# Performance work log

Measured on AMD Instinct MI355X. Metric: run time of the kernel, lower is better.

The kernel has to match this reference:

```python
import jax, jax.numpy as jnp
import numpy as np

B, CIN, COUT, S1, S2, M1, M2 = 16, 64, 64, 128, 128, 16, 16


def _cas(L, dtype):
    # Hartley 'cas' matrix: cos(2*pi*k*k'/L) + sin(2*pi*k*k'/L), symmetric LxL
    k = jnp.arange(L, dtype=dtype)
    ang = (2.0 * jnp.pi / L) * (k[:, None] * k[None, :])
    return jnp.cos(ang) + jnp.sin(ang)


def dht2(x):
    # x: [B, C, M, N] -> dense 2D discrete Hartley transform via matmuls
    M, N = x.shape[-2], x.shape[-1]
    cas_row = _cas(M, x.dtype)
    cas_col = _cas(N, x.dtype)
    # torch: matmul(x, cas_col.T) then matmul(cas_row.T, .)
    y = jnp.einsum('bimn,gn->bimg', x, cas_col)
    return jnp.einsum('mf,bimn->bifn', cas_row, y)


def idht2(x):
    return dht2(x) / (x.shape[-2] * x.shape[-1])


def _neg_freq(a):
    # roll(flip(a, [-1,-2]), (1,1), [-1,-2])
    return jnp.roll(jnp.flip(a, axis=(-2, -1)), shift=(1, 1), axis=(-2, -1))


def compl_mul2d(x1, x2):
    x1n = _neg_freq(x1)
    x2n = _neg_freq(x2)
    e = lambda a, b: jnp.einsum('bixy,ioxy->boxy', a, b)
    return 0.5 * (e(x1, x2) - e(x1n, x2n) + e(x1, x2n) + e(x1n, x2))


def setup_inputs() -> dict:
    key = jax.random.key(0)
    k1, k2, k3 = jax.random.split(key, 3)
    scale = 1.0 / (CIN * COUT)
    x = jax.random.normal(k1, (B, CIN, S1, S2), dtype=jnp.float32)
    weights1 = scale * jax.random.uniform(k2, (CIN, COUT, M1, M2), dtype=jnp.float32)
    weights2 = scale * jax.random.uniform(k3, (CIN, COUT, M1, M2), dtype=jnp.float32)
    return {'x': x, 'weights1': weights1, 'weights2': weights2}


def reference(x, weights1, weights2):
    m1, m2 = weights1.shape[2], weights1.shape[3]
    b, cout = x.shape[0], weights1.shape[1]
    s1, s2 = x.shape[-2], x.shape[-1]

    cos_part = dht2(x)
    sin_part = dht2(jnp.flip(x, axis=(-2, -1)))
    # torch.angle(complex(cos, sin)) == atan2(sin, cos)
    phase = jnp.arctan2(sin_part, cos_part)

    out_dht = jnp.zeros((b, cout, s1, s2), dtype=x.dtype)
    out_dht = out_dht.at[:, :, :m1, :m2].set(
        compl_mul2d(cos_part[:, :, :m1, :m2], weights1))
    out_dht = out_dht.at[:, :, -m1:, :m2].set(
        compl_mul2d(cos_part[:, :, -m1:, :m2], weights2))

    y = idht2(out_dht)
    return y * jnp.cos(phase)
```

## Files before the change

kernel.cpp:

```cpp
#include <hip/hip_runtime.h>

typedef _Float16 f16;
typedef f16 f16x4 __attribute__((ext_vector_type(4)));
typedef f16 f16x8 __attribute__((ext_vector_type(8)));
typedef float f32x4 __attribute__((ext_vector_type(4)));

#define LSCALE 2048.0f
#define LINV   4.8828125e-4f
#define XS 140
#define CS 137

#define MFMA(A,B,C) __builtin_amdgcn_mfma_f32_16x16x32_f16(A, B, C, 0, 0, 0)

__global__ void k_cas(float* __restrict__ casf,
                      f16* __restrict__ Ah, f16* __restrict__ Al,
                      f16* __restrict__ Vh, f16* __restrict__ Vl) {
    int f = blockIdx.x, m = threadIdx.x;
    const float SC = (float)(6.283185307179586 / 128.0);
    float ang = SC * (float)(f * m);
    double a = (double)ang;
    float v = (float)cos(a) + (float)sin(a);
    casf[f * 128 + m] = v;
    f16 h = (f16)v;
    f16 lo = (f16)((v - (float)h) * LSCALE);
    Ah[f * 128 + m] = h;
    Al[f * 128 + m] = lo;
    Vh[f * 128 + 127 - m] = h;
    Vl[f * 128 + 127 - m] = lo;
}

__global__ __launch_bounds__(512, 2) void k_dht(
    const float* __restrict__ xg,
    const f16* __restrict__ Ah, const f16* __restrict__ Al,
    const f16* __restrict__ Vh, const f16* __restrict__ Vl,
    float* __restrict__ cosphi,
    float* __restrict__ cp1, float* __restrict__ cp2)
{
    __shared__ __align__(16) char smem[143360];
    f16* Xh  = (f16*)smem;
    f16* Xl  = (f16*)(smem + 35840);
    f16* W1h = (f16*)smem;
    f16* W1l = (f16*)(smem + 35840);
    f16* W2h = (f16*)(smem + 71680);
    f16* W2l = (f16*)(smem + 107520);
    float* CT = (float*)smem;
    float* ST = (float*)(smem + 70144);

    const int img = blockIdx.x;
    const float* X = xg + (size_t)img * 16384;
    const int t = threadIdx.x;
    const int lane = t & 63;
    const int wv = t >> 6;
    const int l15 = lane & 15;
    const int a4 = lane >> 4;

    #pragma unroll
    for (int it = 0; it < 8; ++it) {
        int i = it * 512 + t;
        int r = i >> 5, c0 = (i & 31) * 4;
        float4 xv = *(const float4*)&X[r * 128 + c0];
        const float* xp = (const float*)&xv;
        f16x4 hv, lv;
        #pragma unroll
        for (int j = 0; j < 4; ++j) {
            f16 h = (f16)xp[j];
            hv[j] = h;
            lv[j] = (f16)((xp[j] - (float)h) * LSCALE);
        }
        *(f16x4*)&Xh[r * XS + c0] = hv;
        *(f16x4*)&Xl[r * XS + c0] = lv;
    }

    f16x8 tAh[4], tAl[4], tVh[4], tVl[4];
    {
        const int row = 16 * wv + l15;
        #pragma unroll
        for (int ks = 0; ks < 4; ++ks) {
            int off = row * 128 + ks * 32 + 8 * a4;
            tAh[ks] = *(const f16x8*)&Ah[off];
            tAl[ks] = *(const f16x8*)&Al[off];
            tVh[ks] = *(const f16x8*)&Vh[off];
            tVl[ks] = *(const f16x8*)&Vl[off];
        }
    }
    __syncthreads();

    f32x4 w1hi[8], w1lo[8], w2hi[8], w2lo[8];
    #pragma unroll
    for (int i = 0; i < 8; ++i) {
        w1hi[i] = (f32x4){0.f,0.f,0.f,0.f}; w1lo[i] = (f32x4){0.f,0.f,0.f,0.f};
        w2hi[i] = (f32x4){0.f,0.f,0.f,0.f}; w2lo[i] = (f32x4){0.f,0.f,0.f,0.f};
    }
    #pragma unroll
    for (int mtp = 0; mtp < 4; ++mtp) {
        #pragma unroll
        for (int ks = 0; ks < 4; ++ks) {
            #pragma unroll
            for (int q = 0; q < 2; ++q) {
                const int mt = 2 * mtp + q;
                const int base = (16 * mt + l15) * XS + ks * 32 + 8 * a4;
                f16x4 h0 = *(const f16x4*)&Xh[base];
                f16x4 h1 = *(const f16x4*)&Xh[base + 4];
                f16x4 l0 = *(const f16x4*)&Xl[base];
                f16x4 l1 = *(const f16x4*)&Xl[base + 4];
                f16x8 xh = __builtin_shufflevector(h0, h1, 0,1,2,3,4,5,6,7);
                f16x8 xl = __builtin_shufflevector(l0, l1, 0,1,2,3,4,5,6,7);
                w1hi[mt] = MFMA(tAh[ks], xh, w1hi[mt]);
                w1lo[mt] = MFMA(tAl[ks], xh, w1lo[mt]);
                w1lo[mt] = MFMA(tAh[ks], xl, w1lo[mt]);
                w2hi[mt] = MFMA(tVh[ks], xh, w2hi[mt]);
                w2lo[mt] = MFMA(tVl[ks], xh, w2lo[mt]);
                w2lo[mt] = MFMA(tVh[ks], xl, w2lo[mt]);
            }
        }
    }
    __syncthreads();

    {
        const int g = 16 * wv + 4 * a4;
        #pragma unroll
        for (int mt = 0; mt < 8; ++mt) {
            const int m = 16 * mt + l15;
            #pragma unroll
            for (int r = 0; r < 4; ++r) {
                float v1 = w1hi[mt][r] + LINV * w1lo[mt][r];
                f16 h1 = (f16)v1;
                W1h[(g + r) * XS + m] = h1;
                W1l[(g + r) * XS + m] = (f16)((v1 - (float)h1) * LSCALE);
                float v2 = w2hi[mt][r] + LINV * w2lo[mt][r];
                f16 h2 = (f16)v2;
                W2h[(g + r) * XS + m] = h2;
                W2l[(g + r) * XS + m] = (f16)((v2 - (float)h2) * LSCALE);
            }
        }
    }
    __syncthreads();

    const int cw  = wv >> 2;
    const int ft0 = 2 * (wv & 3);
    const f16* TBh = cw ? Vh : Ah;
    const f16* TBl = cw ? Vl : Al;
    const f16* Wph = cw ? W2h : W1h;
    const f16* Wpl = cw ? W2l : W1l;

    f16x8 tbh[2][4], tbl[2][4];
    #pragma unroll
    for (int ft = 0; ft < 2; ++ft) {
        const int row = 16 * (ft0 + ft) + l15;
        #pragma unroll
        for (int ks = 0; ks < 4; ++ks) {
            int off = row * 128 + ks * 32 + 8 * a4;
            tbh[ft][ks] = *(const f16x8*)&TBh[off];
            tbl[ft][ks] = *(const f16x8*)&TBl[off];
        }
    }

    f32x4 chi[2][8], clo[2][8];
    #pragma unroll
    for (int ft = 0; ft < 2; ++ft)
        #pragma unroll
        for (int i = 0; i < 8; ++i) {
            chi[ft][i] = (f32x4){0.f,0.f,0.f,0.f};
            clo[ft][i] = (f32x4){0.f,0.f,0.f,0.f};
        }
    #pragma unroll
    for (int gtp = 0; gtp < 4; ++gtp) {
        #pragma unroll
        for (int ks = 0; ks < 4; ++ks) {
            #pragma unroll
            for (int q = 0; q < 2; ++q) {
                const int gt = 2 * gtp + q;
                const int base = (16 * gt + l15) * XS + ks * 32 + 8 * a4;
                f16x4 h0 = *(const f16x4*)&Wph[base];
                f16x4 h1 = *(const f16x4*)&Wph[base + 4];
                f16x4 l0 = *(const f16x4*)&Wpl[base];
                f16x4 l1 = *(const f16x4*)&Wpl[base + 4];
                f16x8 wh = __builtin_shufflevector(h0, h1, 0,1,2,3,4,5,6,7);
                f16x8 wl = __builtin_shufflevector(l0, l1, 0,1,2,3,4,5,6,7);
                #pragma unroll
                for (int ft = 0; ft < 2; ++ft) {
                    chi[ft][gt] = MFMA(wh, tbh[ft][ks], chi[ft][gt]);
                    clo[ft][gt] = MFMA(wl, tbh[ft][ks], clo[ft][gt]);
                    clo[ft][gt] = MFMA(wh, tbl[ft][ks], clo[ft][gt]);
                }
            }
        }
    }
    __syncthreads();

    {
        float* R = cw ? ST : CT;
        const int gg = 4 * a4;
        #pragma unroll
        for (int ft = 0; ft < 2; ++ft) {
            const int f = 16 * (ft0 + ft) + l15;
            #pragma unroll
            for (int gt = 0; gt < 8; ++gt)
                #pragma unroll
                for (int r = 0; r < 4; ++r)
                    R[(16 * gt + gg + r) * CS + f] = chi[ft][gt][r] + LINV * clo[ft][gt][r];
        }
    }
    __syncthreads();

    const int g0 = 4 * (t & 31);
    const int fb = t >> 5;
    const size_t obase = (size_t)img * 16384;
    #pragma unroll
    for (int it = 0; it < 8; ++it) {
        const int f = fb + 16 * it;
        float4 o; float cv[4];
        #pragma unroll
        for (int i = 0; i < 4; ++i) {
            float C = CT[(g0 + i) * CS + f];
            float S = ST[(g0 + i) * CS + f];
            cv[i] = C;
            float d = C * C + S * S;
            ((float*)&o)[i] = (d > 0.f) ? C * rsqrtf(d) : 1.0f;
        }
        *(float4*)&cosphi[obase + f * 128 + g0] = o;
        if (g0 < 16) {
            if (f < 16)
                *(float4*)&cp1[img * 256 + f * 16 + g0] = *(float4*)cv;
            else if (f >= 112)
                *(float4*)&cp2[img * 256 + (f - 112) * 16 + g0] = *(float4*)cv;
        }
    }
}

__global__ __launch_bounds__(256) void k_corner(
    const float* __restrict__ cp1, const float* __restrict__ cp2,
    const float* __restrict__ w1,  const float* __restrict__ w2,
    float* __restrict__ od1, float* __restrict__ od2)
{
    const int c = blockIdx.y;
    const float* cp = c ? cp2 : cp1;
    const float* w  = c ? w2  : w1;
    float* od       = c ? od2 : od1;
    const int b = blockIdx.x >> 6, o = blockIdx.x & 63;
    const int t = threadIdx.x;
    const int xx = t >> 4, yy = t & 15;
    const int nx = (16 - xx) & 15, ny = (16 - yy) & 15;

    float acc = 0.f;
    #pragma unroll 4
    for (int i = 0; i < 64; ++i) {
        float A  = cp[((b * 64 + i) * 16 + xx) * 16 + yy];
        float An = cp[((b * 64 + i) * 16 + nx) * 16 + ny];
        float W  = w[((i * 64 + o) * 16 + xx) * 16 + yy];
        float Wn = w[((i * 64 + o) * 16 + nx) * 16 + ny];
        acc += A * (W + Wn) + An * (W - Wn);
    }
    od[((b * 64 + o) * 16 + xx) * 16 + yy] = 0.5f * acc;
}

__global__ __launch_bounds__(256) void k_inv(
    const float* __restrict__ od1, const float* __restrict__ od2,
    const float* __restrict__ cas,
    float* __restrict__ out)
{
    __shared__ float odS[32 * 16];
    __shared__ float casF[128 * 33];
    __shared__ float Rs[128 * 17];
    __shared__ float casG[16 * 128];

    const int img = blockIdx.x;
    const int t = threadIdx.x;

    odS[t]       = od1[img * 256 + t];
    odS[256 + t] = od2[img * 256 + t];
    #pragma unroll
    for (int k = 0; k < 16; ++k) {
        int idx = t + k * 256;
        int s = idx >> 5, j = idx & 31;
        int f = (j < 16) ? j : (96 + j);
        casF[s * 33 + j] = cas[s * 128 + f];
    }
    #pragma unroll
    for (int k = 0; k < 8; ++k) {
        int idx = t + k * 256;
        casG[idx] = cas[idx];
    }
    __syncthreads();

    {
        const int s1 = t >> 1, gb = (t & 1) * 8;
        float acc[8];
        #pragma unroll
        for (int l = 0; l < 8; ++l) acc[l] = 0.f;
        #pragma unroll 4
        for (int j = 0; j < 32; ++j) {
            float cf = casF[s1 * 33 + j];
            #pragma unroll
            for (int l = 0; l < 8; ++l)
                acc[l] = fmaf(cf, odS[j * 16 + gb + l], acc[l]);
        }
        #pragma unroll
        for (int l = 0; l < 8; ++l) Rs[s1 * 17 + gb + l] = acc[l];
    }
    __syncthreads();

    const float inv = 1.0f / 16384.0f;
    const int grp = t >> 5, lane = t & 31;
    const int s2 = lane * 4;
    for (int r = 0; r < 16; ++r) {
        const int s1 = grp * 16 + r;
        float4 acc = {0.f, 0.f, 0.f, 0.f};
        #pragma unroll
        for (int g = 0; g < 16; ++g) {
            float rv = Rs[s1 * 17 + g];
            float4 c4 = *(const float4*)&casG[g * 128 + s2];
            acc.x = fmaf(rv, c4.x, acc.x);
            acc.y = fmaf(rv, c4.y, acc.y);
            acc.z = fmaf(rv, c4.z, acc.z);
            acc.w = fmaf(rv, c4.w, acc.w);
        }
        size_t idx = (size_t)img * 16384 + (size_t)s1 * 128 + s2;
        float4 ph = *(const float4*)&out[idx];
        float4 res;
        res.x = acc.x * inv * ph.x;
        res.y = acc.y * inv * ph.y;
        res.z = acc.z * inv * ph.z;
        res.w = acc.w * inv * ph.w;
        *(float4*)&out[idx] = res;
    }
}

extern "C" void kernel_launch(void* const* d_in, const int* in_sizes, int n_in,
                              void* d_out, int out_size, void* d_ws, size_t ws_size,
                              hipStream_t stream) {
    (void)in_sizes; (void)n_in; (void)out_size; (void)ws_size;
    const float* x  = (const float*)d_in[0];
    const float* w1 = (const float*)d_in[1];
    const float* w2 = (const float*)d_in[2];
    float* out = (float*)d_out;
    float* ws  = (float*)d_ws;

    float* casf = ws;
    f16* Ah = (f16*)(ws + 16384);
    f16* Al = Ah + 16384;
    f16* Vh = Al + 16384;
    f16* Vl = Vh + 16384;
    float* cp1 = (float*)(Vl + 16384);
    float* cp2 = cp1 + 262144;
    float* od1 = cp2 + 262144;
    float* od2 = od1 + 262144;

    k_cas<<<dim3(128), dim3(128), 0, stream>>>(casf, Ah, Al, Vh, Vl);
    k_dht<<<dim3(1024), dim3(512), 0, stream>>>(x, Ah, Al, Vh, Vl, out, cp1, cp2);
    k_corner<<<dim3(1024, 2), dim3(256), 0, stream>>>(cp1, cp2, w1, w2, od1, od2);
    k_inv<<<dim3(1024), dim3(256), 0, stream>>>(od1, od2, casf, out);
}
```

Measured before the change: 166.1 us.

## Store cos-phase as fp16 directly from MFMA registers with 1024-thread DHT blocks

The DHT kernel now runs 1024 threads per block, splitting work so each wave computes both the cos and sin transforms for its tile. This removes the shared-memory transpose staging of C and S and the extra barriers. The cos(phase) factor is computed straight from the accumulators and written to the output buffer as fp16, halving that intermediate traffic. The inverse kernel stages those fp16 values in shared memory and reads them back. In exchange the phase factor loses precision, the final-stage stores are scattered 2-byte writes, and the inverse kernel uses more LDS, which may cut its occupancy.

```diff
diff --git a/kernel.cpp b/kernel.cpp
--- a/kernel.cpp
+++ b/kernel.cpp
@@ -8,7 +8,6 @@
 #define LSCALE 2048.0f
 #define LINV   4.8828125e-4f
 #define XS 140
-#define CS 137
 
 #define MFMA(A,B,C) __builtin_amdgcn_mfma_f32_16x16x32_f16(A, B, C, 0, 0, 0)
 
@@ -29,11 +28,11 @@
     Vl[f * 128 + 127 - m] = lo;
 }
 
-__global__ __launch_bounds__(512, 2) void k_dht(
+__global__ __launch_bounds__(1024) void k_dht(
     const float* __restrict__ xg,
     const f16* __restrict__ Ah, const f16* __restrict__ Al,
     const f16* __restrict__ Vh, const f16* __restrict__ Vl,
-    float* __restrict__ cosphi,
+    float* __restrict__ outbuf,
     float* __restrict__ cp1, float* __restrict__ cp2)
 {
     __shared__ __align__(16) char smem[143360];
@@ -43,8 +42,6 @@
     f16* W1l = (f16*)(smem + 35840);
     f16* W2h = (f16*)(smem + 71680);
     f16* W2l = (f16*)(smem + 107520);
-    float* CT = (float*)smem;
-    float* ST = (float*)(smem + 70144);
 
     const int img = blockIdx.x;
     const float* X = xg + (size_t)img * 16384;
@@ -55,8 +52,8 @@
     const int a4 = lane >> 4;
 
     #pragma unroll
-    for (int it = 0; it < 8; ++it) {
-        int i = it * 512 + t;
+    for (int it = 0; it < 4; ++it) {
+        int i = it * 1024 + t;
         int r = i >> 5, c0 = (i & 31) * 4;
         float4 xv = *(const float4*)&X[r * 128 + c0];
         const float* xp = (const float*)&xv;
@@ -70,160 +67,124 @@
         *(f16x4*)&Xh[r * XS + c0] = hv;
         *(f16x4*)&Xl[r * XS + c0] = lv;
     }
-
-    f16x8 tAh[4], tAl[4], tVh[4], tVl[4];
-    {
-        const int row = 16 * wv + l15;
-        #pragma unroll
-        for (int ks = 0; ks < 4; ++ks) {
-            int off = row * 128 + ks * 32 + 8 * a4;
-            tAh[ks] = *(const f16x8*)&Ah[off];
-            tAl[ks] = *(const f16x8*)&Al[off];
-            tVh[ks] = *(const f16x8*)&Vh[off];
-            tVl[ks] = *(const f16x8*)&Vl[off];
-        }
-    }
-    __syncthreads();
-
-    f32x4 w1hi[8], w1lo[8], w2hi[8], w2lo[8];
-    #pragma unroll
-    for (int i = 0; i < 8; ++i) {
+    __syncthreads();
+
+    const int gw = wv & 7;
+    const int mh = (wv >> 3) * 4;
+    f32x4 w1hi[4], w1lo[4], w2hi[4], w2lo[4];
+    #pragma unroll
+    for (int i = 0; i < 4; ++i) {
         w1hi[i] = (f32x4){0.f,0.f,0.f,0.f}; w1lo[i] = (f32x4){0.f,0.f,0.f,0.f};
         w2hi[i] = (f32x4){0.f,0.f,0.f,0.f}; w2lo[i] = (f32x4){0.f,0.f,0.f,0.f};
     }
-    #pragma unroll
-    for (int mtp = 0; mtp < 4; ++mtp) {
-        #pragma unroll
+    {
+        const int trow = (16 * gw + l15) * 128;
+        #pragma unroll 1
         for (int ks = 0; ks < 4; ++ks) {
+            const int toff = trow + ks * 32 + 8 * a4;
+            f16x8 tah = *(const f16x8*)&Ah[toff];
+            f16x8 tal = *(const f16x8*)&Al[toff];
+            f16x8 tvh = *(const f16x8*)&Vh[toff];
+            f16x8 tvl = *(const f16x8*)&Vl[toff];
             #pragma unroll
-            for (int q = 0; q < 2; ++q) {
-                const int mt = 2 * mtp + q;
-                const int base = (16 * mt + l15) * XS + ks * 32 + 8 * a4;
+            for (int mi = 0; mi < 4; ++mi) {
+                const int base = (16 * (mh + mi) + l15) * XS + ks * 32 + 8 * a4;
                 f16x4 h0 = *(const f16x4*)&Xh[base];
                 f16x4 h1 = *(const f16x4*)&Xh[base + 4];
                 f16x4 l0 = *(const f16x4*)&Xl[base];
                 f16x4 l1 = *(const f16x4*)&Xl[base + 4];
                 f16x8 xh = __builtin_shufflevector(h0, h1, 0,1,2,3,4,5,6,7);
                 f16x8 xl = __builtin_shufflevector(l0, l1, 0,1,2,3,4,5,6,7);
-                w1hi[mt] = MFMA(tAh[ks], xh, w1hi[mt]);
-                w1lo[mt] = MFMA(tAl[ks], xh, w1lo[mt]);
-                w1lo[mt] = MFMA(tAh[ks], xl, w1lo[mt]);
-                w2hi[mt] = MFMA(tVh[ks], xh, w2hi[mt]);
-                w2lo[mt] = MFMA(tVl[ks], xh, w2lo[mt]);
-                w2lo[mt] = MFMA(tVh[ks], xl, w2lo[mt]);
+                w1hi[mi] = MFMA(tah, xh, w1hi[mi]);
+                w1lo[mi] = MFMA(tal, xh, w1lo[mi]);
+                w1lo[mi] = MFMA(tah, xl, w1lo[mi]);
+                w2hi[mi] = MFMA(tvh, xh, w2hi[mi]);
+                w2lo[mi] = MFMA(tvl, xh, w2lo[mi]);
+                w2lo[mi] = MFMA(tvh, xl, w2lo[mi]);
             }
         }
     }
     __syncthreads();
 
     {
-        const int g = 16 * wv + 4 * a4;
-        #pragma unroll
-        for (int mt = 0; mt < 8; ++mt) {
-            const int m = 16 * mt + l15;
+        const int g = 16 * gw + 4 * a4;
+        #pragma unroll
+        for (int mi = 0; mi < 4; ++mi) {
+            const int m = 16 * (mh + mi) + l15;
             #pragma unroll
             for (int r = 0; r < 4; ++r) {
-                float v1 = w1hi[mt][r] + LINV * w1lo[mt][r];
+                float v1 = w1hi[mi][r] + LINV * w1lo[mi][r];
                 f16 h1 = (f16)v1;
-                W1h[(g + r) * XS + m] = h1;
-                W1l[(g + r) * XS + m] = (f16)((v1 - (float)h1) * LSCALE);
-                float v2 = w2hi[mt][r] + LINV * w2lo[mt][r];
+                float v2 = w2hi[mi][r] + LINV * w2lo[mi][r];
                 f16 h2 = (f16)v2;
                 W2h[(g + r) * XS + m] = h2;
                 W2l[(g + r) * XS + m] = (f16)((v2 - (float)h2) * LSCALE);
+                W1h[(g + r) * XS + m] = h1;
+                W1l[(g + r) * XS + m] = (f16)((v1 - (float)h1) * LSCALE);
             }
         }
     }
     __syncthreads();
 
-    const int cw  = wv >> 2;
-    const int ft0 = 2 * (wv & 3);
-    const f16* TBh = cw ? Vh : Ah;
-    const f16* TBl = cw ? Vl : Al;
-    const f16* Wph = cw ? W2h : W1h;
-    const f16* Wpl = cw ? W2l : W1l;
-
-    f16x8 tbh[2][4], tbl[2][4];
-    #pragma unroll
-    for (int ft = 0; ft < 2; ++ft) {
-        const int row = 16 * (ft0 + ft) + l15;
-        #pragma unroll
+    const int ft = wv >> 1;
+    const int gh = wv & 1;
+    f32x4 chi[4], clo[4], shi[4], slo[4];
+    #pragma unroll
+    for (int i = 0; i < 4; ++i) {
+        chi[i] = (f32x4){0.f,0.f,0.f,0.f}; clo[i] = (f32x4){0.f,0.f,0.f,0.f};
+        shi[i] = (f32x4){0.f,0.f,0.f,0.f}; slo[i] = (f32x4){0.f,0.f,0.f,0.f};
+    }
+    {
+        const int frow = (16 * ft + l15) * 128;
+        #pragma unroll 1
         for (int ks = 0; ks < 4; ++ks) {
-            int off = row * 128 + ks * 32 + 8 * a4;
-            tbh[ft][ks] = *(const f16x8*)&TBh[off];
-            tbl[ft][ks] = *(const f16x8*)&TBl[off];
-        }
-    }
-
-    f32x4 chi[2][8], clo[2][8];
-    #pragma unroll
-    for (int ft = 0; ft < 2; ++ft)
-        #pragma unroll
-        for (int i = 0; i < 8; ++i) {
-            chi[ft][i] = (f32x4){0.f,0.f,0.f,0.f};
-            clo[ft][i] = (f32x4){0.f,0.f,0.f,0.f};
-        }
-    #pragma unroll
-    for (int gtp = 0; gtp < 4; ++gtp) {
-        #pragma unroll
-        for (int ks = 0; ks < 4; ++ks) {
+            const int toff = frow + ks * 32 + 8 * a4;
+            f16x8 tah = *(const f16x8*)&Ah[toff];
+            f16x8 tal = *(const f16x8*)&Al[toff];
+            f16x8 tvh = *(const f16x8*)&Vh[toff];
+            f16x8 tvl = *(const f16x8*)&Vl[toff];
             #pragma unroll
-            for (int q = 0; q < 2; ++q) {
-                const int gt = 2 * gtp + q;
+            for (int gi = 0; gi < 4; ++gi) {
+                const int gt = 4 * gh + gi;
                 const int base = (16 * gt + l15) * XS + ks * 32 + 8 * a4;
-                f16x4 h0 = *(const f16x4*)&Wph[base];
-                f16x4 h1 = *(const f16x4*)&Wph[base + 4];
-                f16x4 l0 = *(const f16x4*)&Wpl[base];
-                f16x4 l1 = *(const f16x4*)&Wpl[base + 4];
-                f16x8 wh = __builtin_shufflevector(h0, h1, 0,1,2,3,4,5,6,7);
-                f16x8 wl = __builtin_shufflevector(l0, l1, 0,1,2,3,4,5,6,7);
-                #pragma unroll
-                for (int ft = 0; ft < 2; ++ft) {
-                    chi[ft][gt] = MFMA(wh, tbh[ft][ks], chi[ft][gt]);
-                    clo[ft][gt] = MFMA(wl, tbh[ft][ks], clo[ft][gt]);
-                    clo[ft][gt] = MFMA(wh, tbl[ft][ks], clo[ft][gt]);
-                }
+                f16x4 ah0 = *(const f16x4*)&W1h[base];
+                f16x4 ah1 = *(const f16x4*)&W1h[base + 4];
+                f16x4 al0 = *(const f16x4*)&W1l[base];
+                f16x4 al1 = *(const f16x4*)&W1l[base + 4];
+                f16x4 bh0 = *(const f16x4*)&W2h[base];
+                f16x4 bh1 = *(const f16x4*)&W2h[base + 4];
+                f16x4 bl0 = *(const f16x4*)&W2l[base];
+                f16x4 bl1 = *(const f16x4*)&W2l[base + 4];
+                f16x8 u1h = __builtin_shufflevector(ah0, ah1, 0,1,2,3,4,5,6,7);
+                f16x8 u1l = __builtin_shufflevector(al0, al1, 0,1,2,3,4,5,6,7);
+                f16x8 u2h = __builtin_shufflevector(bh0, bh1, 0,1,2,3,4,5,6,7);
+                f16x8 u2l = __builtin_shufflevector(bl0, bl1, 0,1,2,3,4,5,6,7);
+                chi[gi] = MFMA(tah, u1h, chi[gi]);
+                clo[gi] = MFMA(tal, u1h, clo[gi]);
+                clo[gi] = MFMA(tah, u1l, clo[gi]);
+                shi[gi] = MFMA(tvh, u2h, shi[gi]);
+                slo[gi] = MFMA(tvl, u2h, slo[gi]);
+                slo[gi] = MFMA(tvh, u2l, slo[gi]);
             }
         }
     }
-    __syncthreads();
-
-    {
-        float* R = cw ? ST : CT;
-        const int gg = 4 * a4;
-        #pragma unroll
-        for (int ft = 0; ft < 2; ++ft) {
-            const int f = 16 * (ft0 + ft) + l15;
-            #pragma unroll
-            for (int gt = 0; gt < 8; ++gt)
-                #pragma unroll
-                for (int r = 0; r < 4; ++r)
-                    R[(16 * gt + gg + r) * CS + f] = chi[ft][gt][r] + LINV * clo[ft][gt][r];
-        }
-    }
-    __syncthreads();
-
-    const int g0 = 4 * (t & 31);
-    const int fb = t >> 5;
-    const size_t obase = (size_t)img * 16384;
-    #pragma unroll
-    for (int it = 0; it < 8; ++it) {
-        const int f = fb + 16 * it;
-        float4 o; float cv[4];
-        #pragma unroll
-        for (int i = 0; i < 4; ++i) {
-            float C = CT[(g0 + i) * CS + f];
-            float S = ST[(g0 + i) * CS + f];
-            cv[i] = C;
-            float d = C * C + S * S;
-            ((float*)&o)[i] = (d > 0.f) ? C * rsqrtf(d) : 1.0f;
-        }
-        *(float4*)&cosphi[obase + f * 128 + g0] = o;
-        if (g0 < 16) {
-            if (f < 16)
-                *(float4*)&cp1[img * 256 + f * 16 + g0] = *(float4*)cv;
-            else if (f >= 112)
-                *(float4*)&cp2[img * 256 + (f - 112) * 16 + g0] = *(float4*)cv;
+
+    f16* cph = (f16*)(outbuf + (size_t)img * 16384);
+    #pragma unroll
+    for (int gi = 0; gi < 4; ++gi) {
+        const int g = 16 * (4 * gh + gi) + l15;
+        #pragma unroll
+        for (int r = 0; r < 4; ++r) {
+            const int f = 16 * ft + 4 * a4 + r;
+            float Cv = chi[gi][r] + LINV * clo[gi][r];
+            float Sv = shi[gi][r] + LINV * slo[gi][r];
+            float d = Cv * Cv + Sv * Sv;
+            float cp = (d > 0.f) ? Cv * rsqrtf(d) : 1.0f;
+            cph[f * 128 + g] = (f16)cp;
+            if (gh == 0 && gi == 0) {
+                if (ft == 0)      cp1[img * 256 + f * 16 + l15] = Cv;
+                else if (ft == 7) cp2[img * 256 + (f - 112) * 16 + l15] = Cv;
+            }
         }
     }
 }
@@ -263,9 +224,17 @@
     __shared__ float casF[128 * 33];
     __shared__ float Rs[128 * 17];
     __shared__ float casG[16 * 128];
+    __shared__ __align__(16) unsigned short cphS[16384];
 
     const int img = blockIdx.x;
     const int t = threadIdx.x;
+
+    const uint4* cp16 = (const uint4*)(out + (size_t)img * 16384);
+    #pragma unroll
+    for (int k = 0; k < 8; ++k) {
+        int i = k * 256 + t;
+        ((uint4*)cphS)[i] = cp16[i];
+    }
 
     odS[t]       = od1[img * 256 + t];
     odS[256 + t] = od2[img * 256 + t];
@@ -315,13 +284,13 @@
             acc.z = fmaf(rv, c4.z, acc.z);
             acc.w = fmaf(rv, c4.w, acc.w);
         }
+        const f16* ph = (const f16*)cphS + s1 * 128 + s2;
         size_t idx = (size_t)img * 16384 + (size_t)s1 * 128 + s2;
-        float4 ph = *(const float4*)&out[idx];
         float4 res;
-        res.x = acc.x * inv * ph.x;
-        res.y = acc.y * inv * ph.y;
-        res.z = acc.z * inv * ph.z;
-        res.w = acc.w * inv * ph.w;
+        res.x = acc.x * inv * (float)ph[0];
+        res.y = acc.y * inv * (float)ph[1];
+        res.z = acc.z * inv * (float)ph[2];
+        res.w = acc.w * inv * (float)ph[3];
         *(float4*)&out[idx] = res;
     }
 }
@@ -347,7 +316,7 @@
     float* od2 = od1 + 262144;
 
     k_cas<<<dim3(128), dim3(128), 0, stream>>>(casf, Ah, Al, Vh, Vl);
-    k_dht<<<dim3(1024), dim3(512), 0, stream>>>(x, Ah, Al, Vh, Vl, out, cp1, cp2);
+    k_dht<<<dim3(1024), dim3(1024), 0, stream>>>(x, Ah, Al, Vh, Vl, out, cp1, cp2);
     k_corner<<<dim3(1024, 2), dim3(256), 0, stream>>>(cp1, cp2, w1, w2, od1, od2);
     k_inv<<<dim3(1024), dim3(256), 0, stream>>>(od1, od2, casf, out);
 }
```

After: 175.7 us. +5.8%, slower.
